# Optimization experiments

Hardware: AMD Instinct MI355X
Metric: run time of the kernel (lower is better)

The kernel has to match this reference:

```python
import jax, jax.numpy as jnp
import numpy as np

IN_DIM, H_DIM, Y_DIM, ROLLOUT = 1024, 2048, 1024, 512


def setup_inputs() -> dict:
    key = jax.random.key(0)
    ks = jax.random.split(key, 4)
    return {
        "x": jax.random.normal(ks[0], (1, ROLLOUT, IN_DIM), dtype=jnp.float32),
        "h": jnp.zeros((H_DIM,), dtype=jnp.float32),
        "Wc": jax.random.normal(ks[1], (IN_DIM + H_DIM, H_DIM), dtype=jnp.float32) * 0.01,
        "Wu": jax.random.normal(ks[2], (IN_DIM + H_DIM, H_DIM), dtype=jnp.float32) * 0.01,
        "bc": jnp.zeros((H_DIM,), dtype=jnp.float32),
        "bu": jnp.zeros((H_DIM,), dtype=jnp.float32),
        "Wh_y": jax.random.normal(ks[3], (H_DIM, Y_DIM), dtype=jnp.float32) * 0.01,
        "by": jnp.zeros((Y_DIM,), dtype=jnp.float32),
    }


def reference(x, h, Wc, Wu, bc, bu, Wh_y, by):
    # x: [1, T, in_dim]; h: [h_dim]. Strict sequential GRU-style cell via scan.
    def step(h_prev, xt):
        xc = jnp.concatenate([xt, h_prev])           # [in+h]
        Lu = jax.nn.sigmoid(xc @ Wu + bu)            # update gate
        c_tilda = jnp.tanh(xc @ Wc + bc)             # candidate
        h_new = Lu * c_tilda + (1.0 - Lu) * h_prev
        y = h_new @ Wh_y + by
        return h_new, y

    h_final, ys = jax.lax.scan(step, h, x[0])        # ys: [T, y_dim]
    return ys, h_final
```

## Files before the change

### kernel.cpp

```cpp
#include <hip/hip_runtime.h>
#include <hip/hip_bf16.h>
#include <math.h>

#define T_STEPS 512
#define IN_DIM  1024
#define H_DIM   2048
#define Y_DIM   1024

#define NBLK2 128
#define BT2   512
#define NWORD (H_DIM / 2)

static __device__ __forceinline__ unsigned f2bf(float f) {
    unsigned u = __float_as_uint(f);
    return ((u + 0x7FFFu + ((u >> 16) & 1u)) >> 16) & 0xFFFFu;
}
static __device__ __forceinline__ float bflo(unsigned p) { return __uint_as_float(p << 16); }
static __device__ __forceinline__ float bfhi(unsigned p) { return __uint_as_float(p & 0xFFFF0000u); }

static __device__ __forceinline__ void sleep_bk(int r) {
    switch (r) {
        case 0: break;
        case 1: __builtin_amdgcn_s_sleep(1); break;
        case 2: __builtin_amdgcn_s_sleep(2); break;
        case 3: __builtin_amdgcn_s_sleep(4); break;
        case 4: __builtin_amdgcn_s_sleep(8); break;
        default: __builtin_amdgcn_s_sleep(16); break;
    }
}

#define TM 64
#define TN 128
#define TK 16

__global__ __launch_bounds__(256) void gemm_bias(
    const float* __restrict__ A, const float* __restrict__ B,
    const float* __restrict__ bias, float* __restrict__ C,
    int M, int N, int K, int lda, int ldb, int ldc)
{
    __shared__ float As[TK][TM + 4];
    __shared__ float Bs[TK][TN + 4];

    const int n0 = blockIdx.x * TN;
    const int m0 = blockIdx.y * TM;
    const int tid = threadIdx.x;
    const int tx = tid & 15;
    const int ty = tid >> 4;

    float acc[4][8] = {};

    for (int k0 = 0; k0 < K; k0 += TK) {
        {
            int mm = tid & 63, kq = tid >> 6;
            float4 a = *(const float4*)&A[(m0 + mm) * lda + k0 + 4 * kq];
            As[4 * kq + 0][mm] = a.x;
            As[4 * kq + 1][mm] = a.y;
            As[4 * kq + 2][mm] = a.z;
            As[4 * kq + 3][mm] = a.w;
        }
        #pragma unroll
        for (int l = tid; l < 512; l += 256) {
            int kk = l >> 5, jj = (l & 31) * 4;
            *(float4*)&Bs[kk][jj] = *(const float4*)&B[(k0 + kk) * ldb + n0 + jj];
        }
        __syncthreads();
        #pragma unroll
        for (int kk = 0; kk < TK; ++kk) {
            float4 a  = *(const float4*)&As[kk][ty * 4];
            float4 b0 = *(const float4*)&Bs[kk][tx * 8];
            float4 b1 = *(const float4*)&Bs[kk][tx * 8 + 4];
            const float av[4] = {a.x, a.y, a.z, a.w};
            const float bv[8] = {b0.x, b0.y, b0.z, b0.w, b1.x, b1.y, b1.z, b1.w};
            #pragma unroll
            for (int r = 0; r < 4; ++r)
                #pragma unroll
                for (int c = 0; c < 8; ++c)
                    acc[r][c] = fmaf(av[r], bv[c], acc[r][c]);
        }
        __syncthreads();
    }

    float4 bv0 = *(const float4*)&bias[n0 + tx * 8];
    float4 bv1 = *(const float4*)&bias[n0 + tx * 8 + 4];
    const float bb[8] = {bv0.x, bv0.y, bv0.z, bv0.w, bv1.x, bv1.y, bv1.z, bv1.w};
    #pragma unroll
    for (int r = 0; r < 4; ++r) {
        float4 o0, o1;
        o0.x = acc[r][0] + bb[0]; o0.y = acc[r][1] + bb[1];
        o0.z = acc[r][2] + bb[2]; o0.w = acc[r][3] + bb[3];
        o1.x = acc[r][4] + bb[4]; o1.y = acc[r][5] + bb[5];
        o1.z = acc[r][6] + bb[6]; o1.w = acc[r][7] + bb[7];
        float* cp = &C[(m0 + ty * 4 + r) * ldc + n0 + tx * 8];
        *(float4*)cp = o0;
        *(float4*)(cp + 4) = o1;
    }
}

__global__ __launch_bounds__(BT2) void gru_seq(
    const float* __restrict__ Wu_h,
    const float* __restrict__ Wc_h,
    const float* __restrict__ XU,
    const float* __restrict__ XC,
    const float* __restrict__ h0,
    unsigned long long* __restrict__ Hp,
    float* __restrict__ H)
{
    __shared__ float hbuf[2][10496];

    const int tid  = threadIdx.x;
    const int w    = tid >> 6;
    const int lane = tid & 63;
    const int jb   = blockIdx.x * 16;
    const int j0   = jb + 2 * w;

    unsigned wru0[16], wru1[16], wrc0[16], wrc1[16];
    #pragma unroll
    for (int q = 0; q < 8; ++q) {
        int e = 4 * (q * 64 + lane);
        const float* u = Wu_h + (size_t)e * H_DIM + j0;
        const float* c = Wc_h + (size_t)e * H_DIM + j0;
        wru0[2*q]   = f2bf(u[0])               | (f2bf(u[(size_t)H_DIM])      << 16);
        wru0[2*q+1] = f2bf(u[2*(size_t)H_DIM]) | (f2bf(u[3*(size_t)H_DIM])    << 16);
        wru1[2*q]   = f2bf(u[1])               | (f2bf(u[(size_t)H_DIM+1])    << 16);
        wru1[2*q+1] = f2bf(u[2*(size_t)H_DIM+1]) | (f2bf(u[3*(size_t)H_DIM+1]) << 16);
        wrc0[2*q]   = f2bf(c[0])               | (f2bf(c[(size_t)H_DIM])      << 16);
        wrc0[2*q+1] = f2bf(c[2*(size_t)H_DIM]) | (f2bf(c[3*(size_t)H_DIM])    << 16);
        wrc1[2*q]   = f2bf(c[1])               | (f2bf(c[(size_t)H_DIM+1])    << 16);
        wrc1[2*q+1] = f2bf(c[2*(size_t)H_DIM+1]) | (f2bf(c[3*(size_t)H_DIM+1]) << 16);
    }

    float hc0 = h0[j0], hc1 = h0[j0 + 1];
    const int myword = blockIdx.x * 8 + w;

    float2 xu_cur = make_float2(0.f, 0.f), xc_cur = make_float2(0.f, 0.f);
    if (lane == 0) {
        xu_cur = *(const float2*)(XU + j0);
        xc_cur = *(const float2*)(XC + j0);
    }

    for (int t = 0; t < T_STEPS; ++t) {
        float2 xu_nxt = make_float2(0.f, 0.f), xc_nxt = make_float2(0.f, 0.f);
        if (lane == 0 && t + 1 < T_STEPS) {
            xu_nxt = *(const float2*)(XU + (size_t)(t + 1) * H_DIM + j0);
            xc_nxt = *(const float2*)(XC + (size_t)(t + 1) * H_DIM + j0);
        }

        float* hb = hbuf[t & 1];

        if (t == 0) {
            *(float4*)&hb[4 * tid] = *(const float4*)&h0[4 * tid];
        } else if (w == 0) {
            const unsigned long long* src = Hp + (size_t)(t - 1) * NWORD;
            const unsigned tag = (unsigned)t;
            unsigned long long v[16];
            #pragma unroll
            for (int i = 0; i < 16; ++i)
                v[i] = __hip_atomic_load(src + i * 64 + lane,
                                         __ATOMIC_RELAXED, __HIP_MEMORY_SCOPE_AGENT);
            unsigned mask = 0;
            #pragma unroll
            for (int i = 0; i < 16; ++i)
                mask |= ((unsigned)(v[i] >> 32) != tag) ? (1u << i) : 0u;

            int rnd = 0;
            while (__any(mask != 0u)) {
                sleep_bk(rnd);
                if (rnd < 5) ++rnd;
                #pragma unroll
                for (int i = 0; i < 16; ++i)
                    if (mask & (1u << i))
                        v[i] = __hip_atomic_load(src + i * 64 + lane,
                                                 __ATOMIC_RELAXED, __HIP_MEMORY_SCOPE_AGENT);
                #pragma unroll
                for (int i = 0; i < 16; ++i)
                    if ((mask & (1u << i)) && (unsigned)(v[i] >> 32) == tag)
                        mask &= ~(1u << i);
            }
            #pragma unroll
            for (int i = 0; i < 16; ++i) {
                unsigned lo = (unsigned)v[i];
                *(float2*)&hb[2 * (i * 64 + lane)] = make_float2(bflo(lo), bfhi(lo));
            }
        }
        __syncthreads();

        float au0 = 0.f, au1 = 0.f, ac0 = 0.f, ac1 = 0.f;
        #pragma unroll
        for (int q = 0; q < 8; ++q) {
            float4 h4 = *(const float4*)&hb[4 * (q * 64 + lane)];
            unsigned a, b;
            a = wru0[2*q]; b = wru0[2*q+1];
            au0 = fmaf(h4.x, bflo(a), au0); au0 = fmaf(h4.y, bfhi(a), au0);
            au0 = fmaf(h4.z, bflo(b), au0); au0 = fmaf(h4.w, bfhi(b), au0);
            a = wru1[2*q]; b = wru1[2*q+1];
            au1 = fmaf(h4.x, bflo(a), au1); au1 = fmaf(h4.y, bfhi(a), au1);
            au1 = fmaf(h4.z, bflo(b), au1); au1 = fmaf(h4.w, bfhi(b), au1);
            a = wrc0[2*q]; b = wrc0[2*q+1];
            ac0 = fmaf(h4.x, bflo(a), ac0); ac0 = fmaf(h4.y, bfhi(a), ac0);
            ac0 = fmaf(h4.z, bflo(b), ac0); ac0 = fmaf(h4.w, bfhi(b), ac0);
            a = wrc1[2*q]; b = wrc1[2*q+1];
            ac1 = fmaf(h4.x, bflo(a), ac1); ac1 = fmaf(h4.y, bfhi(a), ac1);
            ac1 = fmaf(h4.z, bflo(b), ac1); ac1 = fmaf(h4.w, bfhi(b), ac1);
        }
        #pragma unroll
        for (int off = 32; off; off >>= 1) {
            au0 += __shfl_down(au0, off);
            au1 += __shfl_down(au1, off);
            ac0 += __shfl_down(ac0, off);
            ac1 += __shfl_down(ac1, off);
        }

        if (lane == 0) {
            float pu0 = au0 + xu_cur.x, pu1 = au1 + xu_cur.y;
            float pc0 = ac0 + xc_cur.x, pc1 = ac1 + xc_cur.y;
            float ug0 = 1.f / (1.f + __expf(-pu0));
            float ug1 = 1.f / (1.f + __expf(-pu1));
            float e0 = __expf(-2.f * fabsf(pc0));
            float e1 = __expf(-2.f * fabsf(pc1));
            float cg0 = copysignf((1.f - e0) / (1.f + e0), pc0);
            float cg1 = copysignf((1.f - e1) / (1.f + e1), pc1);
            float hn0 = ug0 * cg0 + (1.f - ug0) * hc0;
            float hn1 = ug1 * cg1 + (1.f - ug1) * hc1;
            hc0 = hn0; hc1 = hn1;

            unsigned lo = f2bf(hn0) | (f2bf(hn1) << 16);
            __hip_atomic_store(Hp + (size_t)t * NWORD + myword,
                               ((unsigned long long)(unsigned)(t + 1) << 32) | lo,
                               __ATOMIC_RELAXED, __HIP_MEMORY_SCOPE_AGENT);
            *(float2*)(H + (size_t)t * H_DIM + j0) = make_float2(hn0, hn1);
        }
        xu_cur = xu_nxt; xc_cur = xc_nxt;
    }
}

extern "C" void kernel_launch(void* const* d_in, const int* in_sizes, int n_in,
                              void* d_out, int out_size, void* d_ws, size_t ws_size,
                              hipStream_t stream)
{
    const float* x   = (const float*)d_in[0];
    const float* h0  = (const float*)d_in[1];
    const float* Wc  = (const float*)d_in[2];
    const float* Wu  = (const float*)d_in[3];
    const float* bc  = (const float*)d_in[4];
    const float* bu  = (const float*)d_in[5];
    const float* Why = (const float*)d_in[6];
    const float* by  = (const float*)d_in[7];
    float* out = (float*)d_out;

    float* ws = (float*)d_ws;
    float* XU = ws;
    float* XC = ws + (T_STEPS * H_DIM);
    float* H  = ws + 2 * (T_STEPS * H_DIM);
    unsigned long long* Hp =
        (unsigned long long*)(ws + 3 * (T_STEPS * H_DIM));

    gemm_bias<<<dim3(H_DIM / TN, T_STEPS / TM), 256, 0, stream>>>(
        x, Wu, bu, XU, T_STEPS, H_DIM, IN_DIM, IN_DIM, H_DIM, H_DIM);
    gemm_bias<<<dim3(H_DIM / TN, T_STEPS / TM), 256, 0, stream>>>(
        x, Wc, bc, XC, T_STEPS, H_DIM, IN_DIM, IN_DIM, H_DIM, H_DIM);

    gru_seq<<<NBLK2, BT2, 0, stream>>>(
        Wu + IN_DIM * H_DIM, Wc + IN_DIM * H_DIM, XU, XC, h0, Hp, H);

    gemm_bias<<<dim3(Y_DIM / TN, T_STEPS / TM), 256, 0, stream>>>(
        H, Why, by, out, T_STEPS, Y_DIM, H_DIM, H_DIM, Y_DIM, Y_DIM);

    (void)hipMemcpyAsync(out + T_STEPS * Y_DIM, H + (T_STEPS - 1) * H_DIM,
                         H_DIM * sizeof(float), hipMemcpyDeviceToDevice, stream);
}
```

Baseline: 2.566 ms.

## Fuse output projection into recurrent GRU kernel and shrink GEMM M-tile

Drops the separate output GEMM and the memcpy of the final hidden state. The recurrent kernel now keeps a bf16 slice of Why in shared memory and computes the previous step's y outputs inside each timestep, using warps that would otherwise sit idle. The final step is handled after the loop by polling the published hidden state. The input-projection GEMM tile is halved in M to launch more blocks, at the cost of extra LDS traffic, bf16 rounding of Why, and more work per step on the serial critical path.

Result: faster. 2.371 ms (-7.6%).

```diff
diff --git a/kernel.cpp b/kernel.cpp
--- a/kernel.cpp
+++ b/kernel.cpp
@@ -29,7 +29,7 @@
     }
 }
 
-#define TM 64
+#define TM 32
 #define TN 128
 #define TK 16
 
@@ -47,11 +47,11 @@
     const int tx = tid & 15;
     const int ty = tid >> 4;
 
-    float acc[4][8] = {};
+    float acc[2][8] = {};
 
     for (int k0 = 0; k0 < K; k0 += TK) {
-        {
-            int mm = tid & 63, kq = tid >> 6;
+        if (tid < 128) {
+            int mm = tid & 31, kq = tid >> 5;
             float4 a = *(const float4*)&A[(m0 + mm) * lda + k0 + 4 * kq];
             As[4 * kq + 0][mm] = a.x;
             As[4 * kq + 1][mm] = a.y;
@@ -66,16 +66,15 @@
         __syncthreads();
         #pragma unroll
         for (int kk = 0; kk < TK; ++kk) {
-            float4 a  = *(const float4*)&As[kk][ty * 4];
+            float2 a2 = *(const float2*)&As[kk][ty * 2];
             float4 b0 = *(const float4*)&Bs[kk][tx * 8];
             float4 b1 = *(const float4*)&Bs[kk][tx * 8 + 4];
-            const float av[4] = {a.x, a.y, a.z, a.w};
             const float bv[8] = {b0.x, b0.y, b0.z, b0.w, b1.x, b1.y, b1.z, b1.w};
             #pragma unroll
-            for (int r = 0; r < 4; ++r)
-                #pragma unroll
-                for (int c = 0; c < 8; ++c)
-                    acc[r][c] = fmaf(av[r], bv[c], acc[r][c]);
+            for (int c = 0; c < 8; ++c) {
+                acc[0][c] = fmaf(a2.x, bv[c], acc[0][c]);
+                acc[1][c] = fmaf(a2.y, bv[c], acc[1][c]);
+            }
         }
         __syncthreads();
     }
@@ -84,13 +83,13 @@
     float4 bv1 = *(const float4*)&bias[n0 + tx * 8 + 4];
     const float bb[8] = {bv0.x, bv0.y, bv0.z, bv0.w, bv1.x, bv1.y, bv1.z, bv1.w};
     #pragma unroll
-    for (int r = 0; r < 4; ++r) {
+    for (int r = 0; r < 2; ++r) {
         float4 o0, o1;
         o0.x = acc[r][0] + bb[0]; o0.y = acc[r][1] + bb[1];
         o0.z = acc[r][2] + bb[2]; o0.w = acc[r][3] + bb[3];
         o1.x = acc[r][4] + bb[4]; o1.y = acc[r][5] + bb[5];
         o1.z = acc[r][6] + bb[6]; o1.w = acc[r][7] + bb[7];
-        float* cp = &C[(m0 + ty * 4 + r) * ldc + n0 + tx * 8];
+        float* cp = &C[(m0 + ty * 2 + r) * ldc + n0 + tx * 8];
         *(float4*)cp = o0;
         *(float4*)(cp + 4) = o1;
     }
@@ -102,16 +101,21 @@
     const float* __restrict__ XU,
     const float* __restrict__ XC,
     const float* __restrict__ h0,
+    const float* __restrict__ Why,
+    const float* __restrict__ by,
     unsigned long long* __restrict__ Hp,
-    float* __restrict__ H)
+    float* __restrict__ Y,
+    float* __restrict__ HF)
 {
     __shared__ float hbuf[2][10496];
+    __shared__ unsigned wy[8][1024];
 
     const int tid  = threadIdx.x;
     const int w    = tid >> 6;
     const int lane = tid & 63;
     const int jb   = blockIdx.x * 16;
     const int j0   = jb + 2 * w;
+    const int jy   = blockIdx.x * 8;
 
     unsigned wru0[16], wru1[16], wrc0[16], wrc1[16];
     #pragma unroll
@@ -127,6 +131,19 @@
         wrc0[2*q+1] = f2bf(c[2*(size_t)H_DIM]) | (f2bf(c[3*(size_t)H_DIM])    << 16);
         wrc1[2*q]   = f2bf(c[1])               | (f2bf(c[(size_t)H_DIM+1])    << 16);
         wrc1[2*q+1] = f2bf(c[2*(size_t)H_DIM+1]) | (f2bf(c[3*(size_t)H_DIM+1]) << 16);
+    }
+
+    for (int idx = tid; idx < 8 * 1024; idx += BT2) {
+        int c = idx & 7, p = idx >> 3;
+        wy[c][p] = f2bf(Why[(size_t)(2 * p) * Y_DIM + jy + c]) |
+                   (f2bf(Why[(size_t)(2 * p + 1) * Y_DIM + jy + c]) << 16);
+    }
+
+    const int cA = (w - 1) * 2, cB = cA + 1;
+    float byA = 0.f, byB = 0.f;
+    if (lane == 0 && w >= 1 && w <= 4) {
+        byA = by[jy + cA];
+        byB = by[jy + cB];
     }
 
     float hc0 = h0[j0], hc1 = h0[j0 + 1];
@@ -227,9 +244,97 @@
             __hip_atomic_store(Hp + (size_t)t * NWORD + myword,
                                ((unsigned long long)(unsigned)(t + 1) << 32) | lo,
                                __ATOMIC_RELAXED, __HIP_MEMORY_SCOPE_AGENT);
-            *(float2*)(H + (size_t)t * H_DIM + j0) = make_float2(hn0, hn1);
+            if (t == T_STEPS - 1) {
+                HF[j0]     = hn0;
+                HF[j0 + 1] = hn1;
+            }
+        }
+
+        if (t >= 1 && w >= 1 && w <= 4) {
+            float yA = 0.f, yB = 0.f;
+            #pragma unroll
+            for (int q = 0; q < 8; ++q) {
+                float4 h4 = *(const float4*)&hb[4 * (q * 64 + lane)];
+                int p = 2 * (q * 64 + lane);
+                uint2 wa = *(const uint2*)&wy[cA][p];
+                uint2 wb = *(const uint2*)&wy[cB][p];
+                yA = fmaf(h4.x, bflo(wa.x), yA); yA = fmaf(h4.y, bfhi(wa.x), yA);
+                yA = fmaf(h4.z, bflo(wa.y), yA); yA = fmaf(h4.w, bfhi(wa.y), yA);
+                yB = fmaf(h4.x, bflo(wb.x), yB); yB = fmaf(h4.y, bfhi(wb.x), yB);
+                yB = fmaf(h4.z, bflo(wb.y), yB); yB = fmaf(h4.w, bfhi(wb.y), yB);
+            }
+            #pragma unroll
+            for (int off = 32; off; off >>= 1) {
+                yA += __shfl_down(yA, off);
+                yB += __shfl_down(yB, off);
+            }
+            if (lane == 0) {
+                Y[(size_t)(t - 1) * Y_DIM + jy + cA] = yA + byA;
+                Y[(size_t)(t - 1) * Y_DIM + jy + cB] = yB + byB;
+            }
         }
         xu_cur = xu_nxt; xc_cur = xc_nxt;
+    }
+
+    {
+        float* hb = hbuf[T_STEPS & 1];
+        if (w == 0) {
+            const unsigned long long* src = Hp + (size_t)(T_STEPS - 1) * NWORD;
+            const unsigned tag = (unsigned)T_STEPS;
+            unsigned long long v[16];
+            #pragma unroll
+            for (int i = 0; i < 16; ++i)
+                v[i] = __hip_atomic_load(src + i * 64 + lane,
+                                         __ATOMIC_RELAXED, __HIP_MEMORY_SCOPE_AGENT);
+            unsigned mask = 0;
+            #pragma unroll
+            for (int i = 0; i < 16; ++i)
+                mask |= ((unsigned)(v[i] >> 32) != tag) ? (1u << i) : 0u;
+            int rnd = 0;
+            while (__any(mask != 0u)) {
+                sleep_bk(rnd);
+                if (rnd < 5) ++rnd;
+                #pragma unroll
+                for (int i = 0; i < 16; ++i)
+                    if (mask & (1u << i))
+                        v[i] = __hip_atomic_load(src + i * 64 + lane,
+                                                 __ATOMIC_RELAXED, __HIP_MEMORY_SCOPE_AGENT);
+                #pragma unroll
+                for (int i = 0; i < 16; ++i)
+                    if ((mask & (1u << i)) && (unsigned)(v[i] >> 32) == tag)
+                        mask &= ~(1u << i);
+            }
+            #pragma unroll
+            for (int i = 0; i < 16; ++i) {
+                unsigned lo = (unsigned)v[i];
+                *(float2*)&hb[2 * (i * 64 + lane)] = make_float2(bflo(lo), bfhi(lo));
+            }
+        }
+        __syncthreads();
+
+        if (w >= 1 && w <= 4) {
+            float yA = 0.f, yB = 0.f;
+            #pragma unroll
+            for (int q = 0; q < 8; ++q) {
+                float4 h4 = *(const float4*)&hb[4 * (q * 64 + lane)];
+                int p = 2 * (q * 64 + lane);
+                uint2 wa = *(const uint2*)&wy[cA][p];
+                uint2 wb = *(const uint2*)&wy[cB][p];
+                yA = fmaf(h4.x, bflo(wa.x), yA); yA = fmaf(h4.y, bfhi(wa.x), yA);
+                yA = fmaf(h4.z, bflo(wa.y), yA); yA = fmaf(h4.w, bfhi(wa.y), yA);
+                yB = fmaf(h4.x, bflo(wb.x), yB); yB = fmaf(h4.y, bfhi(wb.x), yB);
+                yB = fmaf(h4.z, bflo(wb.y), yB); yB = fmaf(h4.w, bfhi(wb.y), yB);
+            }
+            #pragma unroll
+            for (int off = 32; off; off >>= 1) {
+                yA += __shfl_down(yA, off);
+                yB += __shfl_down(yB, off);
+            }
+            if (lane == 0) {
+                Y[(size_t)(T_STEPS - 1) * Y_DIM + jy + cA] = yA + byA;
+                Y[(size_t)(T_STEPS - 1) * Y_DIM + jy + cB] = yB + byB;
+            }
+        }
     }
 }
 
@@ -250,9 +355,8 @@
     float* ws = (float*)d_ws;
     float* XU = ws;
     float* XC = ws + (T_STEPS * H_DIM);
-    float* H  = ws + 2 * (T_STEPS * H_DIM);
     unsigned long long* Hp =
-        (unsigned long long*)(ws + 3 * (T_STEPS * H_DIM));
+        (unsigned long long*)(ws + 2 * (T_STEPS * H_DIM));
 
     gemm_bias<<<dim3(H_DIM / TN, T_STEPS / TM), 256, 0, stream>>>(
         x, Wu, bu, XU, T_STEPS, H_DIM, IN_DIM, IN_DIM, H_DIM, H_DIM);
@@ -260,11 +364,6 @@
         x, Wc, bc, XC, T_STEPS, H_DIM, IN_DIM, IN_DIM, H_DIM, H_DIM);
 
     gru_seq<<<NBLK2, BT2, 0, stream>>>(
-        Wu + IN_DIM * H_DIM, Wc + IN_DIM * H_DIM, XU, XC, h0, Hp, H);
-
-    gemm_bias<<<dim3(Y_DIM / TN, T_STEPS / TM), 256, 0, stream>>>(
-        H, Why, by, out, T_STEPS, Y_DIM, H_DIM, H_DIM, Y_DIM, Y_DIM);
-
-    (void)hipMemcpyAsync(out + T_STEPS * Y_DIM, H + (T_STEPS - 1) * H_DIM,
-                         H_DIM * sizeof(float), hipMemcpyDeviceToDevice, stream);
-}
+        Wu + IN_DIM * H_DIM, Wc + IN_DIM * H_DIM, XU, XC, h0, Why, by,
+        Hp, out, out + (size_t)T_STEPS * Y_DIM);
+}
```
